# Kernel tuning notes

Measured on AMD Instinct MI355X. Metric: run time of the kernel, lower is better.

## Reference

```python
import jax, jax.numpy as jnp
import numpy as np

K = 1.0        # Lorentz curvature parameter
SQRT_K = 1.0
B, E, T = 128, 64, 2048
F1, D, F2, NC = 16, 2, 32, 4


def linner(u, v):
    # Lorentz inner product <u,v>_L over the last axis (time component first)
    return -u[..., :1] * v[..., :1] + jnp.sum(u[..., 1:] * v[..., 1:], axis=-1, keepdims=True)


def add_time(space):
    # manifold.add_time / projx: time = sqrt(K + ||space||^2)
    t = jnp.sqrt(K + jnp.sum(space * space, axis=-1, keepdims=True))
    return jnp.concatenate([t, space], axis=-1)


def conv2d(x, w, padding, groups=1):
    return jax.lax.conv_general_dilated(
        x, w, window_strides=(1, 1), padding=padding,
        dimension_numbers=('NCHW', 'OIHW', 'NCHW'), feature_group_count=groups)


def bn2d(x, gamma, beta, eps=1e-3):
    # BatchNorm2d (training-mode batch statistics, eps=0.001)
    mean = jnp.mean(x, axis=(0, 2, 3), keepdims=True)
    var = jnp.var(x, axis=(0, 2, 3), keepdims=True)
    return (x - mean) * jax.lax.rsqrt(var + eps) * gamma.reshape(1, -1, 1, 1) + beta.reshape(1, -1, 1, 1)


def avgpool_w(x, k=4):
    # torch AvgPool2d((1,k), stride=k), floor mode
    Wo = x.shape[-1] // k
    return jnp.mean(x[..., :Wo * k].reshape(x.shape[:-1] + (Wo, k)), axis=-1)


def lorentz_bn(x, s, eps=1e-5):
    # AdaMom-style Riemannian batch norm on the hyperboloid (eta=1 -> pure batch stats,
    # learn_mean=False -> target mean is origin, learn_std=True -> learnable scale s).
    C = x.shape[-1]
    o = jnp.zeros((C,), x.dtype).at[0].set(SQRT_K)                      # origin
    avg = jnp.mean(x, axis=0, keepdims=True)
    mu = SQRT_K * avg / jnp.sqrt(jnp.maximum(-linner(avg, avg), 1e-8))  # batch centroid
    xin = -linner(x, mu)                                                # >= K on manifold
    dist = SQRT_K * jnp.arccosh(jnp.maximum(xin / K, 1.0 + 1e-7))
    u = x - (xin / K) * mu                                              # log_mu direction
    v = dist * u / jnp.sqrt(jnp.maximum(linner(u, u), 1e-8))            # log_mu(x)
    var = jnp.mean(dist * dist, axis=0, keepdims=True)                  # scalar dispersion
    v = v + (linner(o, v) / (K - linner(mu, o))) * (mu + o)             # PT mu -> origin
    v = v * (s.reshape(1, 1, -1, 1) / jnp.sqrt(var + eps))
    n = jnp.sqrt(jnp.maximum(linner(v, v), 1e-9))
    return jnp.cosh(n / SQRT_K) * o + SQRT_K * jnp.sinh(n / SQRT_K) * v / n  # exp_origin


def lorentz_avgpool_w(x, k=4):
    # window mean followed by Lorentz centroid renormalization
    Bb, H, W, C = x.shape
    Wo = W // k
    avg = jnp.mean(x[:, :, :Wo * k, :].reshape(Bb, H, Wo, k, C), axis=3)
    return SQRT_K * avg / jnp.sqrt(jnp.maximum(-linner(avg, avg), 1e-8))


def lorentz_flatten(x):
    Bb, H, W, C = x.shape
    t = x[..., 0].reshape(Bb, -1)
    s = x[..., 1:].reshape(Bb, -1)
    t_new = jnp.sqrt(jnp.maximum(jnp.sum(t * t, axis=-1, keepdims=True) - (H * W - 1) * K, 1e-8))
    return jnp.concatenate([t_new, s], axis=-1)


def lorentz_mlr(x, a, z):
    inv = 1.0 / SQRT_K
    norm_z = jnp.linalg.norm(z, axis=-1)                                  # (NC,)
    w_t = jnp.sinh(inv * a) * norm_z
    beta = jnp.sqrt(jnp.maximum((jnp.cosh(inv * a) * norm_z) ** 2 - w_t ** 2, 1e-8))
    alpha = -x[:, :1] * w_t[None, :] + jnp.cosh(inv * a)[None, :] * (x[:, 1:] @ z.T)
    d = SQRT_K * jnp.abs(jnp.arcsinh(inv * alpha / beta[None, :]))
    return jnp.sign(alpha) * beta[None, :] * d


def setup_inputs():
    key = jax.random.key(0)
    ks = jax.random.split(key, 8)
    Cin = F1 * D + 1   # 33
    Cout = F2 + 1      # 33
    feat = F2 * 128    # flattened space dim: W 2049 -> 512 -> 513 -> 128
    return {
        'inputs': jax.random.normal(ks[0], (B, E, T), jnp.float32),
        'domains': jax.random.randint(ks[1], (B,), 0, 4, jnp.int32),
        'conv1_w': jax.random.normal(ks[2], (F1, 1, 1, 32), jnp.float32) / np.float32(np.sqrt(32.0)),
        'bn1_gamma': jnp.ones((F1,), jnp.float32),
        'bn1_beta': jnp.zeros((F1,), jnp.float32),
        'conv2_w': jax.random.normal(ks[3], (F1 * D, 1, E, 1), jnp.float32) / np.float32(np.sqrt(E)),
        'bn2_gamma': jnp.ones((F1 * D,), jnp.float32),
        'bn2_beta': jnp.zeros((F1 * D,), jnp.float32),
        'ec1_w': jax.random.normal(ks[4], (F1 * D, 1, 1, 16), jnp.float32) / np.float32(np.sqrt(16.0)),
        'lc1_w': jax.random.normal(ks[5], (Cout, Cin), jnp.float32) / np.float32(np.sqrt(Cin)),
        'bn_s': jnp.ones((513,), jnp.float32),
        'mlr_a': jax.random.normal(ks[6], (NC,), jnp.float32) * 0.01,
        'mlr_z': jax.random.normal(ks[7], (NC, feat), jnp.float32) * 0.01,
    }


def reference(inputs, domains, conv1_w, bn1_gamma, bn1_beta, conv2_w, bn2_gamma, bn2_beta,
              ec1_w, lc1_w, bn_s, mlr_a, mlr_z):
    x = inputs[:, None, :, :]                           # (B,1,E,T)
    x = conv2d(x, conv1_w, [(0, 0), (16, 16)])          # (B,16,64,2049)
    x = bn2d(x, bn1_gamma, bn1_beta)
    x = conv2d(x, conv2_w, [(0, 0), (0, 0)], groups=F1) # (B,32,1,2049) depthwise over electrodes
    x = bn2d(x, bn2_gamma, bn2_beta)
    x = jax.nn.elu(x)
    x = avgpool_w(x)                                    # (B,32,1,512)  (dropout = eval no-op)
    x = conv2d(x, ec1_w, [(0, 0), (8, 8)], groups=F1 * D)  # (B,32,1,513)
    x = jnp.transpose(x, (0, 2, 3, 1))                  # (B,1,513,32) channels-last
    x = x / (jnp.linalg.norm(x, axis=-1, keepdims=True) + 1e-8)
    x = add_time(x)                                     # projx(pad(x, (1,0))) -> (B,1,513,33)
    # LorentzConv2d 1x1 (kernel_len=1): clamp time, linear, recompute time from space output
    pre = jnp.concatenate([jnp.maximum(x[..., :1], SQRT_K), x[..., 1:]], axis=-1)
    y = jnp.einsum('bhwi,oi->bhwo', pre, lc1_w)
    x = add_time(y[..., 1:])
    x = lorentz_bn(x, bn_s)
    x = add_time(jax.nn.elu(x[..., 1:]))                # LorentzeLU
    x = lorentz_avgpool_w(x)                            # (B,1,128,33)
    feats = lorentz_flatten(x)                          # (B, 4097)
    logits = lorentz_mlr(feats, mlr_a, mlr_z)           # (B, 4)
    return logits, feats
```

## Files before the change

### kernel.cpp

```cpp
#include <hip/hip_runtime.h>
#include <math.h>

#define BB 128
#define EE 64
#define TT 2048
#define C2 32
#define W1 2049
#define WPW 512
#define FEAT 4096
#define NBLK 1024

#define OFF_P    ((size_t)0)
#define OFF_X2   ((size_t)4194304)
#define OFF_PSUM ((size_t)8388608)
#define OFF_PSQ  ((size_t)8421376)
#define OFF_SS   ((size_t)8454144)
#define OFF_H    ((size_t)8454208)
#define OFF_QSQ  ((size_t)10616896)
#define OFF_G    ((size_t)10633280)

__device__ __forceinline__ unsigned short f2b(float f) {
    unsigned int u = __float_as_uint(f);
    u += 0x7FFFu + ((u >> 16) & 1u);
    return (unsigned short)(u >> 16);
}
__device__ __forceinline__ float b2f(unsigned short s) {
    return __uint_as_float(((unsigned int)s) << 16);
}
__device__ __forceinline__ float elu_fast(float a) {
    return (a > 0.f) ? a : (__expf(a) - 1.f);
}

__global__ __launch_bounds__(256) void k_p(const float* __restrict__ in,
        const float* __restrict__ w2, unsigned short* __restrict__ P) {
    int b = blockIdx.y, t0 = blockIdx.x * 256, tid = threadIdx.x;
    __shared__ unsigned short li[64][256];
    __shared__ float lw2s[32][64];
    const float* ib = in + (size_t)b * EE * TT + t0;
    for (int j = tid; j < 64 * 64; j += 256) {
        int e = j >> 6, q = j & 63;
        float4 v = *(const float4*)(ib + e * TT + q * 4);
        li[e][q * 4 + 0] = f2b(v.x); li[e][q * 4 + 1] = f2b(v.y);
        li[e][q * 4 + 2] = f2b(v.z); li[e][q * 4 + 3] = f2b(v.w);
    }
    for (int j = tid; j < 2048; j += 256) lw2s[j >> 6][j & 63] = w2[j];
    __syncthreads();
    int cg = tid >> 6, colg = tid & 63;
    int c8 = cg * 8;
    float acc[4][8];
#pragma unroll
    for (int x = 0; x < 4; x++)
#pragma unroll
        for (int jj = 0; jj < 8; jj++) acc[x][jj] = 0.f;
    for (int e = 0; e < 64; e += 2) {
        uint2 r0 = *(const uint2*)&li[e][colg * 4];
        uint2 r1 = *(const uint2*)&li[e + 1][colg * 4];
        float v0[4], v1[4];
        v0[0] = __uint_as_float(r0.x << 16); v0[1] = __uint_as_float(r0.x & 0xFFFF0000u);
        v0[2] = __uint_as_float(r0.y << 16); v0[3] = __uint_as_float(r0.y & 0xFFFF0000u);
        v1[0] = __uint_as_float(r1.x << 16); v1[1] = __uint_as_float(r1.x & 0xFFFF0000u);
        v1[2] = __uint_as_float(r1.y << 16); v1[3] = __uint_as_float(r1.y & 0xFFFF0000u);
#pragma unroll
        for (int jj = 0; jj < 8; jj++) {
            float2 wv = *(const float2*)&lw2s[c8 + jj][e];
#pragma unroll
            for (int x = 0; x < 4; x++) {
                acc[x][jj] = fmaf(wv.x, v0[x], acc[x][jj]);
                acc[x][jj] = fmaf(wv.y, v1[x], acc[x][jj]);
            }
        }
    }
    unsigned short* Pb = P + (size_t)b * C2 * TT + t0 + colg * 4;
#pragma unroll
    for (int jj = 0; jj < 8; jj++) {
        int c = c8 + jj;
        uint2 o;
        o.x = (unsigned int)f2b(acc[0][jj]) | ((unsigned int)f2b(acc[1][jj]) << 16);
        o.y = (unsigned int)f2b(acc[2][jj]) | ((unsigned int)f2b(acc[3][jj]) << 16);
        *(uint2*)(Pb + (size_t)c * TT) = o;
    }
}

__global__ __launch_bounds__(256) void k_cs(const unsigned short* __restrict__ P,
        const float* __restrict__ w1, const float* __restrict__ g1,
        unsigned short* __restrict__ x2, float* __restrict__ psum, float* __restrict__ psq) {
    int bx = blockIdx.x, b = blockIdx.y, w0 = bx * 256, tid = threadIdx.x;
    __shared__ unsigned short lp[32][288];
    __shared__ float lw1[16][32];
    __shared__ float lds_s[32], lds_q[32];
    const unsigned short* Pb = P + (size_t)b * C2 * TT;
    for (int j = tid; j < 32 * 72; j += 256) {
        int c = j / 72, g4 = j % 72;
        int t = w0 - 16 + g4 * 4;
        uint2 v = make_uint2(0u, 0u);
        if (t >= 0 && t + 3 < TT) v = *(const uint2*)(Pb + (size_t)c * TT + t);
        *(uint2*)&lp[c][g4 * 4] = v;
    }
    for (int j = tid; j < 512; j += 256) {
        int g = j >> 5;
        float sgn = (g1[g] < 0.f) ? -1.f : 1.f;
        lw1[g][j & 31] = w1[j] * sgn;
    }
    __syncthreads();
    for (int r = 0; r < 8; r++) {
        int task = r * 256 + tid;
        int c = task >> 6;
        int wq = task & 63;
        int wbase = wq * 4;
        float win[36];
#pragma unroll
        for (int i = 0; i < 9; i++) {
            uint2 v = *(const uint2*)&lp[c][wbase + i * 4];
            win[i * 4 + 0] = __uint_as_float(v.x << 16);
            win[i * 4 + 1] = __uint_as_float(v.x & 0xFFFF0000u);
            win[i * 4 + 2] = __uint_as_float(v.y << 16);
            win[i * 4 + 3] = __uint_as_float(v.y & 0xFFFF0000u);
        }
        const float* wc = lw1[c >> 1];
        float ls = 0.f, lq = 0.f;
        float accs[4];
#pragma unroll
        for (int i = 0; i < 4; i++) {
            float acc = 0.f;
#pragma unroll
            for (int k = 0; k < 32; k++) acc = fmaf(wc[k], win[i + k], acc);
            accs[i] = acc;
            ls += acc; lq = fmaf(acc, acc, lq);
        }
        uint2 o;
        o.x = (unsigned int)f2b(accs[0]) | ((unsigned int)f2b(accs[1]) << 16);
        o.y = (unsigned int)f2b(accs[2]) | ((unsigned int)f2b(accs[3]) << 16);
        *(uint2*)(x2 + ((size_t)b * C2 + c) * TT + w0 + wbase) = o;
#pragma unroll
        for (int d = 1; d < 64; d <<= 1) {
            ls += __shfl_xor(ls, d);
            lq += __shfl_xor(lq, d);
        }
        if ((tid & 63) == 0) { lds_s[c] = ls; lds_q[c] = lq; }
    }
    __syncthreads();
    if (bx == 7 && tid < 32) {
        const float* wc = lw1[tid >> 1];
        float acc = 0.f;
#pragma unroll
        for (int k = 0; k < 16; k++) acc = fmaf(wc[k], b2f(lp[tid][256 + k]), acc);
        lds_s[tid] += acc;
        lds_q[tid] += acc * acc;
    }
    __syncthreads();
    if (tid < 32) {
        int blk = b * 8 + bx;
        psum[tid * NBLK + blk] = lds_s[tid];
        psq[tid * NBLK + blk]  = lds_q[tid];
    }
}

__global__ __launch_bounds__(64) void k_bn2fin(
        const float* __restrict__ psum, const float* __restrict__ psq,
        const float* __restrict__ gamma, const float* __restrict__ beta,
        float* __restrict__ ss) {
    int c = blockIdx.x, l = threadIdx.x;
    float s = 0.f, q = 0.f;
    for (int j = l; j < NBLK; j += 64) { s += psum[c * NBLK + j]; q += psq[c * NBLK + j]; }
#pragma unroll
    for (int d = 1; d < 64; d <<= 1) { s += __shfl_xor(s, d); q += __shfl_xor(q, d); }
    if (l == 0) {
        float n = (float)(BB * W1);
        float m = s / n;
        float var = q / n - m * m;
        float sc = gamma[c] * rsqrtf(var + 1e-3f);
        ss[c] = sc;
        ss[32 + c] = beta[c] - m * sc;
    }
}

__global__ __launch_bounds__(256) void k_mid(
        const unsigned short* __restrict__ x2, const float* __restrict__ ss,
        const float* __restrict__ ew, const float* __restrict__ lc1,
        float* __restrict__ H) {
    int b = blockIdx.y, w0 = blockIdx.x * 64, tid = threadIdx.x;
    __shared__ __align__(16) float ly[32][82];
    __shared__ float lss[64];
    __shared__ float lew[32][17];
    __shared__ __align__(16) float lxn[8][8][32];
    if (tid < 64) lss[tid] = ss[tid];
    for (int j = tid; j < 512; j += 256) lew[j >> 4][j & 15] = ew[j];
    __syncthreads();
    const unsigned short* xb = x2 + (size_t)b * C2 * TT;
    for (int it = 0; it < 10; it++) {
        int idx = it * 256 + tid;
        int c = idx / 80, q = idx - c * 80;
        int ty = w0 - 8 + q;
        float r = 0.f;
        if (ty >= 0 && ty < WPW) {
            uint2 v = *(const uint2*)(xb + (size_t)c * TT + ty * 4);
            float sc = lss[c], sh = lss[32 + c];
            float a0 = elu_fast(fmaf(sc, __uint_as_float(v.x << 16), sh));
            float a1 = elu_fast(fmaf(sc, __uint_as_float(v.x & 0xFFFF0000u), sh));
            float a2 = elu_fast(fmaf(sc, __uint_as_float(v.y << 16), sh));
            float a3 = elu_fast(fmaf(sc, __uint_as_float(v.y & 0xFFFF0000u), sh));
            r = (a0 + a1 + a2 + a3) * 0.25f;
        }
        ly[c][q] = r;
    }
    __syncthreads();
    int c = tid & 31, wl = tid >> 5;
    float win[24];
#pragma unroll
    for (int m = 0; m < 12; m++) {
        float2 v = *(const float2*)&ly[c][wl * 8 + m * 2];
        win[m * 2] = v.x; win[m * 2 + 1] = v.y;
    }
    float wc[16];
#pragma unroll
    for (int k = 0; k < 16; k++) wc[k] = lew[c][k];
    float acc[8];
#pragma unroll
    for (int i = 0; i < 8; i++) {
        float a = 0.f;
#pragma unroll
        for (int k = 0; k < 16; k++) a = fmaf(wc[k], win[i + k], a);
        acc[i] = a;
    }
    float ss8[8];
#pragma unroll
    for (int i = 0; i < 8; i++) ss8[i] = acc[i] * acc[i];
#pragma unroll
    for (int d = 1; d < 32; d <<= 1) {
#pragma unroll
        for (int i = 0; i < 8; i++) ss8[i] += __shfl_xor(ss8[i], d);
    }
    float pre0[8];
#pragma unroll
    for (int i = 0; i < 8; i++) {
        float inv = 1.f / (sqrtf(ss8[i]) + 1e-8f);
        lxn[wl][i][c] = acc[i] * inv;
        float s2 = ss8[i] * inv * inv;
        pre0[i] = fmaxf(sqrtf(1.f + s2), 1.f);
    }
    float wt0 = lc1[(c + 1) * 33];
    float wreg[32];
#pragma unroll
    for (int k = 0; k < 32; k++) wreg[k] = lc1[(c + 1) * 33 + 1 + k];
    float y8[8];
#pragma unroll
    for (int i = 0; i < 8; i++) {
        float y = wt0 * pre0[i];
#pragma unroll
        for (int q = 0; q < 8; q++) {
            float4 xv = *(const float4*)&lxn[wl][i][q * 4];
            y = fmaf(wreg[q * 4 + 0], xv.x, y);
            y = fmaf(wreg[q * 4 + 1], xv.y, y);
            y = fmaf(wreg[q * 4 + 2], xv.z, y);
            y = fmaf(wreg[q * 4 + 3], xv.w, y);
        }
        y8[i] = y;
    }
    float sy8[8];
#pragma unroll
    for (int i = 0; i < 8; i++) sy8[i] = y8[i] * y8[i];
#pragma unroll
    for (int d = 1; d < 32; d <<= 1) {
#pragma unroll
        for (int i = 0; i < 8; i++) sy8[i] += __shfl_xor(sy8[i], d);
    }
#pragma unroll
    for (int i = 0; i < 8; i++) {
        int w = w0 + wl * 8 + i;
        float* hrow = H + ((size_t)w * BB + b) * 33;
        hrow[1 + c] = y8[i];
        if (c == 0) hrow[0] = sqrtf(1.f + sy8[i]);
    }
}

__global__ __launch_bounds__(256) void k_tail2(
        const float* __restrict__ H, const float* __restrict__ bs,
        float* __restrict__ G) {
    int w = blockIdx.x;
    int tid = threadIdx.x;
    int l = tid & 1, b = tid >> 1;
    int wv = tid >> 6;
    __shared__ float wsum[4][2][17];
    __shared__ float vsum[4];
    float x[17];
    const float* hp = H + ((size_t)w * BB + b) * 33;
#pragma unroll
    for (int k = 0; k < 17; k++) {
        int ch = 2 * k + l;
        x[k] = (ch < 33) ? hp[ch] : 0.f;
    }
    float mu[17];
#pragma unroll
    for (int k = 0; k < 17; k++) mu[k] = x[k];
#pragma unroll
    for (int d = 2; d < 64; d <<= 1) {
#pragma unroll
        for (int k = 0; k < 17; k++) mu[k] += __shfl_xor(mu[k], d);
    }
    if ((tid & 63) < 2) {
#pragma unroll
        for (int k = 0; k < 17; k++) wsum[wv][tid & 1][k] = mu[k];
    }
    __syncthreads();
#pragma unroll
    for (int k = 0; k < 17; k++)
        mu[k] = (wsum[0][l][k] + wsum[1][l][k] + wsum[2][l][k] + wsum[3][l][k]) * (1.f / 128.f);
    float a0 = (l == 0) ? mu[0] : 0.f;
    a0 += __shfl_xor(a0, 1);
    float spp = 0.f;
#pragma unroll
    for (int k = 0; k < 17; k++) spp = fmaf(mu[k], mu[k], spp);
    if (l == 0) spp -= 2.f * mu[0] * mu[0];
    spp += __shfl_xor(spp, 1);
    float rd = rsqrtf(fmaxf(-spp, 1e-8f));
#pragma unroll
    for (int k = 0; k < 17; k++) mu[k] *= rd;
    float mu0 = a0 * rd;
    float pp = 0.f;
#pragma unroll
    for (int k = 0; k < 17; k++) pp = fmaf(x[k], mu[k], pp);
    if (l == 0) pp -= 2.f * x[0] * mu[0];
    pp += __shfl_xor(pp, 1);
    float xin = -pp;
    float dist = acoshf(fmaxf(xin, 1.f + 1e-7f));
    float dq = dist * dist;
#pragma unroll
    for (int d = 2; d < 64; d <<= 1) dq += __shfl_xor(dq, d);
    if ((tid & 63) == 0) vsum[wv] = dq;
    __syncthreads();
    float var = (vsum[0] + vsum[1] + vsum[2] + vsum[3]) * (1.f / 128.f);
#pragma unroll
    for (int k = 0; k < 17; k++) x[k] = x[k] - xin * mu[k];
    float lup = 0.f;
#pragma unroll
    for (int k = 0; k < 17; k++) lup = fmaf(x[k], x[k], lup);
    if (l == 0) lup -= 2.f * x[0] * x[0];
    lup += __shfl_xor(lup, 1);
    float f = dist * rsqrtf(fmaxf(lup, 1e-8f));
#pragma unroll
    for (int k = 0; k < 17; k++) x[k] *= f;
    float v0 = (l == 0) ? x[0] : 0.f;
    v0 += __shfl_xor(v0, 1);
    float corr = -v0 / (1.f + mu0);
#pragma unroll
    for (int k = 0; k < 17; k++) x[k] = fmaf(corr, mu[k], x[k]);
    if (l == 0) x[0] += corr;
    float scb = bs[w] * rsqrtf(var + 1e-5f);
#pragma unroll
    for (int k = 0; k < 17; k++) x[k] *= scb;
    float nnp = 0.f;
#pragma unroll
    for (int k = 0; k < 17; k++) nnp = fmaf(x[k], x[k], nnp);
    if (l == 0) nnp -= 2.f * x[0] * x[0];
    nnp += __shfl_xor(nnp, 1);
    float n = sqrtf(fmaxf(nnp, 1e-9f));
    float shn = sinhf(n) / n;
    float e[17];
#pragma unroll
    for (int k = 0; k < 17; k++) e[k] = elu_fast(shn * x[k]);
    float sgp = 0.f;
#pragma unroll
    for (int k = 0; k < 17; k++) sgp = fmaf(e[k], e[k], sgp);
    if (l == 0) sgp -= e[0] * e[0];
    sgp += __shfl_xor(sgp, 1);
    float g0 = sqrtf(1.f + sgp);
    float* gp = G + ((size_t)w * BB + b) * 33;
#pragma unroll
    for (int k = 0; k < 17; k++) {
        int ch = 2 * k + l;
        if (ch >= 1 && ch < 33) gp[ch] = e[k];
    }
    if (l == 0) gp[0] = g0;
}

__global__ __launch_bounds__(256) void k_pool(
        const float* __restrict__ G, float* __restrict__ outp,
        float* __restrict__ qsq) {
    int item = blockIdx.x * 256 + threadIdx.x;
    int wp = item >> 7, b = item & 127;
    float avg[33];
#pragma unroll
    for (int ch = 0; ch < 33; ch++) avg[ch] = 0.f;
    for (int j = 0; j < 4; j++) {
        const float* gp = G + ((size_t)(wp * 4 + j) * BB + b) * 33;
#pragma unroll
        for (int ch = 0; ch < 33; ch++) avg[ch] += gp[ch];
    }
#pragma unroll
    for (int ch = 0; ch < 33; ch++) avg[ch] *= 0.25f;
    float sp2 = 0.f;
#pragma unroll
    for (int i = 1; i < 33; i++) sp2 = fmaf(avg[i], avg[i], sp2);
    float lnr = avg[0] * avg[0] - sp2;
    float rd2 = rsqrtf(fmaxf(lnr, 1e-8f));
    float q0 = avg[0] * rd2;
    float* fb = outp + 512 + (size_t)b * 4097;
#pragma unroll
    for (int i = 1; i < 33; i++) fb[1 + wp * 32 + (i - 1)] = avg[i] * rd2;
    qsq[b * 128 + wp] = q0 * q0;
}

__global__ __launch_bounds__(256) void k_mlr2(
        const float* __restrict__ qsq, const float* __restrict__ z,
        const float* __restrict__ a, float* __restrict__ outp) {
    int b = blockIdx.x, tid = threadIdx.x;
    __shared__ float red[4][8];
    __shared__ float tnsh;
    if (tid < 64) {
        float s = qsq[b * 128 + tid] + qsq[b * 128 + 64 + tid];
#pragma unroll
        for (int d = 1; d < 64; d <<= 1) s += __shfl_xor(s, d);
        if (tid == 0) tnsh = sqrtf(fmaxf(s - 127.f, 1e-8f));
    }
    __syncthreads();
    float tn = tnsh;
    const float* fs = outp + 512 + (size_t)b * 4097 + 1;
    float sdot[4] = {0.f, 0.f, 0.f, 0.f}, sq[4] = {0.f, 0.f, 0.f, 0.f};
    for (int i = tid * 4; i < FEAT; i += 1024) {
        float f0 = fs[i], f1 = fs[i + 1], f2 = fs[i + 2], f3 = fs[i + 3];
#pragma unroll
        for (int c = 0; c < 4; c++) {
            float4 zv = *(const float4*)(z + c * FEAT + i);
            sdot[c] = fmaf(f0, zv.x, sdot[c]); sdot[c] = fmaf(f1, zv.y, sdot[c]);
            sdot[c] = fmaf(f2, zv.z, sdot[c]); sdot[c] = fmaf(f3, zv.w, sdot[c]);
            sq[c] = fmaf(zv.x, zv.x, sq[c]); sq[c] = fmaf(zv.y, zv.y, sq[c]);
            sq[c] = fmaf(zv.z, zv.z, sq[c]); sq[c] = fmaf(zv.w, zv.w, sq[c]);
        }
    }
#pragma unroll
    for (int d = 1; d < 64; d <<= 1) {
#pragma unroll
        for (int c = 0; c < 4; c++) {
            sdot[c] += __shfl_xor(sdot[c], d);
            sq[c]   += __shfl_xor(sq[c], d);
        }
    }
    int wv = tid >> 6;
    if ((tid & 63) == 0) {
#pragma unroll
        for (int c = 0; c < 4; c++) { red[wv][c] = sdot[c]; red[wv][4 + c] = sq[c]; }
    }
    __syncthreads();
    if (tid == 0) {
        outp[512 + (size_t)b * 4097] = tn;
#pragma unroll
        for (int c = 0; c < 4; c++) {
            float dot = red[0][c] + red[1][c] + red[2][c] + red[3][c];
            float qz  = red[0][4 + c] + red[1][4 + c] + red[2][4 + c] + red[3][4 + c];
            float nz = sqrtf(qz);
            float ca = coshf(a[c]), sa = sinhf(a[c]);
            float wt = sa * nz;
            float cb = ca * nz;
            float bb = sqrtf(fmaxf(cb * cb - wt * wt, 1e-8f));
            float alpha = fmaf(-tn, wt, ca * dot);
            float d = fabsf(asinhf(alpha / bb));
            float sg = (alpha > 0.f) ? 1.f : ((alpha < 0.f) ? -1.f : 0.f);
            outp[b * 4 + c] = sg * bb * d;
        }
    }
}

extern "C" void kernel_launch(void* const* d_in, const int* in_sizes, int n_in,
                              void* d_out, int out_size, void* d_ws, size_t ws_size,
                              hipStream_t stream) {
    const float* in   = (const float*)d_in[0];
    const float* w1   = (const float*)d_in[2];
    const float* g1   = (const float*)d_in[3];
    const float* w2   = (const float*)d_in[5];
    const float* g2   = (const float*)d_in[6];
    const float* b2   = (const float*)d_in[7];
    const float* ew   = (const float*)d_in[8];
    const float* lc1  = (const float*)d_in[9];
    const float* bs   = (const float*)d_in[10];
    const float* mlra = (const float*)d_in[11];
    const float* mlrz = (const float*)d_in[12];
    float* out = (float*)d_out;
    float* ws = (float*)d_ws;

    unsigned short* P  = (unsigned short*)(ws + OFF_P);
    unsigned short* X2 = (unsigned short*)(ws + OFF_X2);
    float* PSUM = ws + OFF_PSUM;
    float* PSQ  = ws + OFF_PSQ;
    float* SS   = ws + OFF_SS;
    float* H    = ws + OFF_H;
    float* QSQ  = ws + OFF_QSQ;
    float* G    = ws + OFF_G;

    k_p<<<dim3(8, 128), 256, 0, stream>>>(in, w2, P);
    k_cs<<<dim3(8, 128), 256, 0, stream>>>(P, w1, g1, X2, PSUM, PSQ);
    k_bn2fin<<<32, 64, 0, stream>>>(PSUM, PSQ, g2, b2, SS);
    k_mid<<<dim3(8, 128), 256, 0, stream>>>(X2, SS, ew, lc1, H);
    k_tail2<<<512, 256, 0, stream>>>(H, bs, G);
    k_pool<<<64, 256, 0, stream>>>(G, out, QSQ);
    k_mlr2<<<128, 256, 0, stream>>>(QSQ, mlrz, mlra, out);
}
```

Measured before the change: 202.2 us.

## Stream fp32 input directly in k_p, widen k_mid loads, fuse pool and MLR

```diff
diff --git a/kernel.cpp b/kernel.cpp
--- a/kernel.cpp
+++ b/kernel.cpp
@@ -16,7 +16,6 @@
 #define OFF_PSQ  ((size_t)8421376)
 #define OFF_SS   ((size_t)8454144)
 #define OFF_H    ((size_t)8454208)
-#define OFF_QSQ  ((size_t)10616896)
 #define OFF_G    ((size_t)10633280)
 
 __device__ __forceinline__ unsigned short f2b(float f) {
@@ -34,16 +33,11 @@
 __global__ __launch_bounds__(256) void k_p(const float* __restrict__ in,
         const float* __restrict__ w2, unsigned short* __restrict__ P) {
     int b = blockIdx.y, t0 = blockIdx.x * 256, tid = threadIdx.x;
-    __shared__ unsigned short li[64][256];
-    __shared__ float lw2s[32][64];
-    const float* ib = in + (size_t)b * EE * TT + t0;
-    for (int j = tid; j < 64 * 64; j += 256) {
-        int e = j >> 6, q = j & 63;
-        float4 v = *(const float4*)(ib + e * TT + q * 4);
-        li[e][q * 4 + 0] = f2b(v.x); li[e][q * 4 + 1] = f2b(v.y);
-        li[e][q * 4 + 2] = f2b(v.z); li[e][q * 4 + 3] = f2b(v.w);
-    }
-    for (int j = tid; j < 2048; j += 256) lw2s[j >> 6][j & 63] = w2[j];
+    __shared__ float lw2t[64][32];
+    for (int j = tid; j < 2048; j += 256) {
+        int e = j >> 5, c = j & 31;
+        lw2t[e][c] = w2[c * 64 + e];
+    }
     __syncthreads();
     int cg = tid >> 6, colg = tid & 63;
     int c8 = cg * 8;
@@ -52,23 +46,19 @@
     for (int x = 0; x < 4; x++)
 #pragma unroll
         for (int jj = 0; jj < 8; jj++) acc[x][jj] = 0.f;
-    for (int e = 0; e < 64; e += 2) {
-        uint2 r0 = *(const uint2*)&li[e][colg * 4];
-        uint2 r1 = *(const uint2*)&li[e + 1][colg * 4];
-        float v0[4], v1[4];
-        v0[0] = __uint_as_float(r0.x << 16); v0[1] = __uint_as_float(r0.x & 0xFFFF0000u);
-        v0[2] = __uint_as_float(r0.y << 16); v0[3] = __uint_as_float(r0.y & 0xFFFF0000u);
-        v1[0] = __uint_as_float(r1.x << 16); v1[1] = __uint_as_float(r1.x & 0xFFFF0000u);
-        v1[2] = __uint_as_float(r1.y << 16); v1[3] = __uint_as_float(r1.y & 0xFFFF0000u);
-#pragma unroll
-        for (int jj = 0; jj < 8; jj++) {
-            float2 wv = *(const float2*)&lw2s[c8 + jj][e];
-#pragma unroll
-            for (int x = 0; x < 4; x++) {
-                acc[x][jj] = fmaf(wv.x, v0[x], acc[x][jj]);
-                acc[x][jj] = fmaf(wv.y, v1[x], acc[x][jj]);
-            }
-        }
+    const float* ibase = in + (size_t)b * EE * TT + t0 + colg * 4;
+#pragma unroll 4
+    for (int e = 0; e < 64; e++) {
+        float4 iv = *(const float4*)(ibase + (size_t)e * TT);
+        float4 wa = *(const float4*)&lw2t[e][c8];
+        float4 wb = *(const float4*)&lw2t[e][c8 + 4];
+        float cv[4] = {iv.x, iv.y, iv.z, iv.w};
+        float wv[8] = {wa.x, wa.y, wa.z, wa.w, wb.x, wb.y, wb.z, wb.w};
+#pragma unroll
+        for (int jj = 0; jj < 8; jj++)
+#pragma unroll
+            for (int x = 0; x < 4; x++)
+                acc[x][jj] = fmaf(wv[jj], cv[x], acc[x][jj]);
     }
     unsigned short* Pb = P + (size_t)b * C2 * TT + t0 + colg * 4;
 #pragma unroll
@@ -187,21 +177,25 @@
     for (int j = tid; j < 512; j += 256) lew[j >> 4][j & 15] = ew[j];
     __syncthreads();
     const unsigned short* xb = x2 + (size_t)b * C2 * TT;
-    for (int it = 0; it < 10; it++) {
+    for (int it = 0; it < 5; it++) {
         int idx = it * 256 + tid;
-        int c = idx / 80, q = idx - c * 80;
-        int ty = w0 - 8 + q;
-        float r = 0.f;
+        int c = idx / 40, m = idx - c * 40;
+        int ty = w0 - 8 + 2 * m;
+        float r0 = 0.f, r1 = 0.f;
         if (ty >= 0 && ty < WPW) {
-            uint2 v = *(const uint2*)(xb + (size_t)c * TT + ty * 4);
+            uint4 v = *(const uint4*)(xb + (size_t)c * TT + ty * 4);
             float sc = lss[c], sh = lss[32 + c];
-            float a0 = elu_fast(fmaf(sc, __uint_as_float(v.x << 16), sh));
-            float a1 = elu_fast(fmaf(sc, __uint_as_float(v.x & 0xFFFF0000u), sh));
-            float a2 = elu_fast(fmaf(sc, __uint_as_float(v.y << 16), sh));
-            float a3 = elu_fast(fmaf(sc, __uint_as_float(v.y & 0xFFFF0000u), sh));
-            r = (a0 + a1 + a2 + a3) * 0.25f;
-        }
-        ly[c][q] = r;
+            r0 = (elu_fast(fmaf(sc, __uint_as_float(v.x << 16), sh))
+                + elu_fast(fmaf(sc, __uint_as_float(v.x & 0xFFFF0000u), sh))
+                + elu_fast(fmaf(sc, __uint_as_float(v.y << 16), sh))
+                + elu_fast(fmaf(sc, __uint_as_float(v.y & 0xFFFF0000u), sh))) * 0.25f;
+            r1 = (elu_fast(fmaf(sc, __uint_as_float(v.z << 16), sh))
+                + elu_fast(fmaf(sc, __uint_as_float(v.z & 0xFFFF0000u), sh))
+                + elu_fast(fmaf(sc, __uint_as_float(v.w << 16), sh))
+                + elu_fast(fmaf(sc, __uint_as_float(v.w & 0xFFFF0000u), sh))) * 0.25f;
+        }
+        ly[c][2 * m] = r0;
+        ly[c][2 * m + 1] = r1;
     }
     __syncthreads();
     int c = tid & 31, wl = tid >> 5;
@@ -373,58 +367,57 @@
     if (l == 0) gp[0] = g0;
 }
 
-__global__ __launch_bounds__(256) void k_pool(
-        const float* __restrict__ G, float* __restrict__ outp,
-        float* __restrict__ qsq) {
-    int item = blockIdx.x * 256 + threadIdx.x;
-    int wp = item >> 7, b = item & 127;
-    float avg[33];
-#pragma unroll
-    for (int ch = 0; ch < 33; ch++) avg[ch] = 0.f;
-    for (int j = 0; j < 4; j++) {
-        const float* gp = G + ((size_t)(wp * 4 + j) * BB + b) * 33;
-#pragma unroll
-        for (int ch = 0; ch < 33; ch++) avg[ch] += gp[ch];
-    }
-#pragma unroll
-    for (int ch = 0; ch < 33; ch++) avg[ch] *= 0.25f;
-    float sp2 = 0.f;
-#pragma unroll
-    for (int i = 1; i < 33; i++) sp2 = fmaf(avg[i], avg[i], sp2);
-    float lnr = avg[0] * avg[0] - sp2;
-    float rd2 = rsqrtf(fmaxf(lnr, 1e-8f));
-    float q0 = avg[0] * rd2;
-    float* fb = outp + 512 + (size_t)b * 4097;
-#pragma unroll
-    for (int i = 1; i < 33; i++) fb[1 + wp * 32 + (i - 1)] = avg[i] * rd2;
-    qsq[b * 128 + wp] = q0 * q0;
-}
-
-__global__ __launch_bounds__(256) void k_mlr2(
-        const float* __restrict__ qsq, const float* __restrict__ z,
+__global__ __launch_bounds__(256) void k_pm(
+        const float* __restrict__ G, const float* __restrict__ z,
         const float* __restrict__ a, float* __restrict__ outp) {
     int b = blockIdx.x, tid = threadIdx.x;
+    __shared__ float feats[128 * 33];
+    __shared__ float qs[128];
     __shared__ float red[4][8];
     __shared__ float tnsh;
+    if (tid < 128) {
+        int wp = tid;
+        float avg[33];
+#pragma unroll
+        for (int ch = 0; ch < 33; ch++) avg[ch] = 0.f;
+        for (int j = 0; j < 4; j++) {
+            const float* gp = G + ((size_t)(wp * 4 + j) * BB + b) * 33;
+#pragma unroll
+            for (int ch = 0; ch < 33; ch++) avg[ch] += gp[ch];
+        }
+#pragma unroll
+        for (int ch = 0; ch < 33; ch++) avg[ch] *= 0.25f;
+        float sp2 = 0.f;
+#pragma unroll
+        for (int i = 1; i < 33; i++) sp2 = fmaf(avg[i], avg[i], sp2);
+        float lnr = avg[0] * avg[0] - sp2;
+        float rd2 = rsqrtf(fmaxf(lnr, 1e-8f));
+        float q0 = avg[0] * rd2;
+        qs[wp] = q0 * q0;
+#pragma unroll
+        for (int i = 1; i < 33; i++) feats[wp * 33 + (i - 1)] = avg[i] * rd2;
+    }
+    __syncthreads();
     if (tid < 64) {
-        float s = qsq[b * 128 + tid] + qsq[b * 128 + 64 + tid];
+        float s = qs[tid] + qs[tid + 64];
 #pragma unroll
         for (int d = 1; d < 64; d <<= 1) s += __shfl_xor(s, d);
         if (tid == 0) tnsh = sqrtf(fmaxf(s - 127.f, 1e-8f));
     }
     __syncthreads();
     float tn = tnsh;
-    const float* fs = outp + 512 + (size_t)b * 4097 + 1;
+    float* fb = outp + 512 + (size_t)b * 4097;
+    for (int i = tid; i < 4096; i += 256) fb[1 + i] = feats[i + (i >> 5)];
+    if (tid == 0) fb[0] = tn;
     float sdot[4] = {0.f, 0.f, 0.f, 0.f}, sq[4] = {0.f, 0.f, 0.f, 0.f};
-    for (int i = tid * 4; i < FEAT; i += 1024) {
-        float f0 = fs[i], f1 = fs[i + 1], f2 = fs[i + 2], f3 = fs[i + 3];
+    for (int k = 0; k < 16; k++) {
+        int j = tid + k * 256;
+        float fv = feats[j + (j >> 5)];
 #pragma unroll
         for (int c = 0; c < 4; c++) {
-            float4 zv = *(const float4*)(z + c * FEAT + i);
-            sdot[c] = fmaf(f0, zv.x, sdot[c]); sdot[c] = fmaf(f1, zv.y, sdot[c]);
-            sdot[c] = fmaf(f2, zv.z, sdot[c]); sdot[c] = fmaf(f3, zv.w, sdot[c]);
-            sq[c] = fmaf(zv.x, zv.x, sq[c]); sq[c] = fmaf(zv.y, zv.y, sq[c]);
-            sq[c] = fmaf(zv.z, zv.z, sq[c]); sq[c] = fmaf(zv.w, zv.w, sq[c]);
+            float zv = z[c * FEAT + j];
+            sdot[c] = fmaf(fv, zv, sdot[c]);
+            sq[c]   = fmaf(zv, zv, sq[c]);
         }
     }
 #pragma unroll
@@ -442,7 +435,6 @@
     }
     __syncthreads();
     if (tid == 0) {
-        outp[512 + (size_t)b * 4097] = tn;
 #pragma unroll
         for (int c = 0; c < 4; c++) {
             float dot = red[0][c] + red[1][c] + red[2][c] + red[3][c];
@@ -483,7 +475,6 @@
     float* PSQ  = ws + OFF_PSQ;
     float* SS   = ws + OFF_SS;
     float* H    = ws + OFF_H;
-    float* QSQ  = ws + OFF_QSQ;
     float* G    = ws + OFF_G;
 
     k_p<<<dim3(8, 128), 256, 0, stream>>>(in, w2, P);
@@ -491,6 +482,5 @@
     k_bn2fin<<<32, 64, 0, stream>>>(PSUM, PSQ, g2, b2, SS);
     k_mid<<<dim3(8, 128), 256, 0, stream>>>(X2, SS, ew, lc1, H);
     k_tail2<<<512, 256, 0, stream>>>(H, bs, G);
-    k_pool<<<64, 256, 0, stream>>>(G, out, QSQ);
-    k_mlr2<<<128, 256, 0, stream>>>(QSQ, mlrz, mlra, out);
-}
+    k_pm<<<128, 256, 0, stream>>>(G, mlrz, mlra, out);
+}
```

New measurement: 203.4 us. Within noise of the previous version (+0.6%).
